# Kernel tuning notes

Hardware: AMD Instinct MI355X
Metric: run time of the kernel (lower is better)

## Reference

```python
import jax, jax.numpy as jnp
import numpy as np

N, E, E2 = 50000, 100000, 100000
NODE_IN, H, EDGE_IN, EDGE_H = 64, 32, 16, 128
STEPS = 3
ALPHA = 0.5
BETA = 1.0 / STEPS  # forward overwrites self.beta with 1/num_steps
EPS = 1e-5


def setup_inputs() -> dict:
    key = jax.random.key(0)
    ks = jax.random.split(key, 16)
    p = lambda k, shape, s=0.05: (jax.random.normal(k, shape, jnp.float32) * s)
    return {
        "n_feat": jax.random.normal(ks[0], (N, NODE_IN), jnp.float32),
        "e_feat": jax.random.normal(ks[1], (E, EDGE_IN), jnp.float32),
        "src": jax.random.randint(ks[2], (E,), 0, N, jnp.int32),
        "dst": jax.random.randint(ks[3], (E,), 0, N, jnp.int32),
        "src_list": jax.random.randint(ks[4], (E2,), 0, N, jnp.int32),
        "dst_list": jax.random.randint(ks[5], (E2,), 0, N, jnp.int32),
        "lin0_w": p(ks[6], (H, NODE_IN)), "lin0_b": jnp.zeros((H,), jnp.float32),
        "en1_w": p(ks[7], (EDGE_H, EDGE_IN)), "en1_b": jnp.zeros((EDGE_H,), jnp.float32),
        "en2_w": p(ks[8], (H * H, EDGE_H)), "en2_b": jnp.zeros((H * H,), jnp.float32),
        "conv_bias": jnp.zeros((H,), jnp.float32),
        "lin1_w": p(ks[9], (H, H)), "lin1_b": jnp.zeros((H,), jnp.float32),
        "bn_gamma": jnp.ones((H,), jnp.float32), "bn_beta": jnp.zeros((H,), jnp.float32),
        "ylin_w": p(ks[10], (3, H)), "ylin_b": jnp.zeros((3,), jnp.float32),
        "ylin2_w": p(ks[11], (1, H)), "ylin2_b": jnp.zeros((1,), jnp.float32),
    }


def reference(n_feat, e_feat, src, dst, src_list, dst_list,
              lin0_w, lin0_b, en1_w, en1_b, en2_w, en2_b, conv_bias,
              lin1_w, lin1_b, bn_gamma, bn_beta, ylin_w, ylin_b, ylin2_w, ylin2_b):
    n = n_feat.shape[0]
    out = jax.nn.relu(n_feat @ lin0_w.T + lin0_b)
    h0 = out
    # Edge-conditioned weights (eval mode: dropouts are identity, so the
    # edge MLP output is identical every step -> compute once).
    We = (jax.nn.relu(e_feat @ en1_w.T + en1_b) @ en2_w.T + en2_b).reshape(-1, H, H)  # (E,H,H)
    for _ in range(STEPS):
        msg = jnp.einsum('eh,eho->eo', out[src], We)                 # per-edge matvec
        agg = jax.ops.segment_sum(msg, dst, num_segments=n)          # sum aggregator
        conv = agg + out + conv_bias                                 # identity residual + bias
        temp = ALPHA * conv + (1.0 - ALPHA) * h0
        out = jax.nn.relu(BETA * (temp @ lin1_w.T + lin1_b) + (1.0 - BETA) * temp)
    # BatchNorm1d with batch statistics (training-mode stats, biased var)
    mu = out.mean(axis=0)
    var = ((out - mu) ** 2).mean(axis=0)
    y_bn = (out - mu) / jnp.sqrt(var + EPS) * bn_gamma + bn_beta
    y_sigmoid = jax.nn.sigmoid(y_bn @ ylin_w.T + ylin_b)                              # (N,3)
    edge_hop_out = jax.nn.sigmoid((y_bn[src_list] * y_bn[dst_list]) @ ylin2_w.T + ylin2_b)  # (E2,1)
    return (y_sigmoid, edge_hop_out)
```

## Files before the change

kernel.cpp:

```cpp
#include <hip/hip_runtime.h>
#include <hip/hip_bf16.h>
#include <math.h>

#define HH 32
#define NODE_IN 64
#define EDGE_IN 16
#define EDGE_H 128
#define M_TILE 256

typedef __attribute__((ext_vector_type(8))) short bf16x8;
typedef __attribute__((ext_vector_type(4))) float f32x4;

__device__ inline unsigned short f2bf(float f) {
    union { float f; unsigned int u; } v; v.f = f;
    unsigned int r = v.u + 0x7fff + ((v.u >> 16) & 1);
    return (unsigned short)(r >> 16);
}

__device__ inline void gload_lds16(const void* g, void* lds) {
    __builtin_amdgcn_global_load_lds(
        (const __attribute__((address_space(1))) void*)g,
        (__attribute__((address_space(3))) void*)lds, 16, 0, 0);
}

__global__ void k_prep_w2(const float* __restrict__ en2_w, unsigned short* __restrict__ W2s) {
    int i = blockIdx.x * 256 + threadIdx.x;
    int r = i >> 7, q = i & 127;
    int p = q >> 3, sub = q & 7;
    int c = p ^ (r & 15);
    W2s[i] = f2bf(en2_w[r * EDGE_H + c * 8 + sub]);
}

__global__ void __launch_bounds__(256, 4)
k_prep_r(const float* __restrict__ e_feat, const float* __restrict__ en1_w,
         const float* __restrict__ en1_b, unsigned short* __restrict__ Rb,
         int E, int E_pad) {
    int t = threadIdx.x, wave = t >> 6, l = t & 63;
    int lo = l & 15, lq = l >> 4;
    int ebase = blockIdx.x * 256 + wave * 64;

    bf16x8 bfrag[8];
    #pragma unroll
    for (int nt = 0; nt < 8; ++nt) {
        unsigned short br[8] = {0, 0, 0, 0, 0, 0, 0, 0};
        if (lq < 2) {
            const float* wr = en1_w + (nt * 16 + lo) * EDGE_IN + lq * 8;
            #pragma unroll
            for (int z = 0; z < 8; ++z) br[z] = f2bf(wr[z]);
        }
        bfrag[nt] = *(const bf16x8*)br;
    }
    float b1v[8];
    #pragma unroll
    for (int nt = 0; nt < 8; ++nt) b1v[nt] = en1_b[nt * 16 + lo];

    #pragma unroll
    for (int m = 0; m < 4; ++m) {
        int ea = ebase + m * 16 + lo;
        unsigned short ar[8] = {0, 0, 0, 0, 0, 0, 0, 0};
        if (lq < 2 && ea < E) {
            const float* er = e_feat + (size_t)ea * EDGE_IN + lq * 8;
            float4 v0 = ((const float4*)er)[0];
            float4 v1 = ((const float4*)er)[1];
            ar[0] = f2bf(v0.x); ar[1] = f2bf(v0.y); ar[2] = f2bf(v0.z); ar[3] = f2bf(v0.w);
            ar[4] = f2bf(v1.x); ar[5] = f2bf(v1.y); ar[6] = f2bf(v1.z); ar[7] = f2bf(v1.w);
        }
        bf16x8 af = *(const bf16x8*)ar;

        int erow = ebase + m * 16 + lq * 4;
        #pragma unroll
        for (int nt = 0; nt < 8; ++nt) {
            f32x4 acc = (f32x4){b1v[nt], b1v[nt], b1v[nt], b1v[nt]};
            acc = __builtin_amdgcn_mfma_f32_16x16x32_bf16(af, bfrag[nt], acc, 0, 0, 0);
            #pragma unroll
            for (int r = 0; r < 4; ++r)
                Rb[(size_t)(erow + r) * EDGE_H + nt * 16 + lo] = f2bf(fmaxf(acc[r], 0.f));
        }
    }
}

__global__ void k_lin0(const float* __restrict__ nf, const float* __restrict__ w,
                       const float* __restrict__ b, float* __restrict__ out,
                       float* __restrict__ h0, int n) {
    __shared__ float nf_s[8][NODE_IN];
    __shared__ float w_s[HH][NODE_IN + 1];
    int t = threadIdx.x;
    for (int i = t; i < HH * NODE_IN; i += 256) w_s[i / NODE_IN][i % NODE_IN] = w[i];
    int n0 = blockIdx.x * 8;
    for (int i = t; i < 8 * NODE_IN; i += 256) {
        int nl = i / NODE_IN, k = i % NODE_IN;
        int nn = n0 + nl;
        nf_s[nl][k] = (nn < n) ? nf[(size_t)nn * NODE_IN + k] : 0.f;
    }
    __syncthreads();
    int nl = t >> 5, h = t & 31;
    int nn = n0 + nl;
    if (nn < n) {
        float acc = b[h];
        #pragma unroll
        for (int k = 0; k < NODE_IN; ++k) acc += nf_s[nl][k] * w_s[h][k];
        acc = fmaxf(acc, 0.f);
        out[(size_t)nn * HH + h] = acc;
        h0[(size_t)nn * HH + h] = acc;
    }
}

__global__ void k_zero_int(int* __restrict__ p, int n) {
    int i = blockIdx.x * 256 + threadIdx.x;
    if (i < n) p[i] = 0;
}
__global__ void k_hist(const int* __restrict__ dst, int* __restrict__ deg, int E) {
    int e = blockIdx.x * 256 + threadIdx.x;
    if (e < E) atomicAdd(&deg[dst[e]], 1);
}
__global__ void k_scan1(const int* __restrict__ deg, int* __restrict__ offtmp,
                        int* __restrict__ bsum, int n) {
    __shared__ int sh[256];
    int tid = threadIdx.x;
    int i = blockIdx.x * 256 + tid;
    int v = (i < n) ? deg[i] : 0;
    sh[tid] = v;
    __syncthreads();
    for (int d = 1; d < 256; d <<= 1) {
        int add = (tid >= d) ? sh[tid - d] : 0;
        __syncthreads();
        sh[tid] += add;
        __syncthreads();
    }
    if (i < n) offtmp[i] = sh[tid] - v;
    if (tid == 255) bsum[blockIdx.x] = sh[255];
}
__global__ void k_scan2(int* __restrict__ bsum, int nb) {
    __shared__ int sh[256];
    int tid = threadIdx.x;
    int v = (tid < nb) ? bsum[tid] : 0;
    sh[tid] = v;
    __syncthreads();
    for (int d = 1; d < 256; d <<= 1) {
        int add = (tid >= d) ? sh[tid - d] : 0;
        __syncthreads();
        sh[tid] += add;
        __syncthreads();
    }
    if (tid < nb) bsum[tid] = sh[tid] - v;
}
__global__ void k_scan3(const int* __restrict__ offtmp, const int* __restrict__ bsum,
                        int* __restrict__ offsets, int* __restrict__ cursor, int n, int E) {
    int i = blockIdx.x * 256 + threadIdx.x;
    if (i < n) { offsets[i] = offtmp[i] + bsum[i >> 8]; cursor[i] = 0; }
    if (i == n) offsets[n] = E;
}
__global__ void k_scatter_pos(const int* __restrict__ dst, const int* __restrict__ offsets,
                              int* __restrict__ cursor, int* __restrict__ pos, int E) {
    int e = blockIdx.x * 256 + threadIdx.x;
    if (e < E) pos[e] = offsets[dst[e]] + atomicAdd(&cursor[dst[e]], 1);
}

__global__ void __launch_bounds__(512, 2)
k_edge_mfma4(const unsigned short* __restrict__ Rb, const unsigned short* __restrict__ W2s,
             const float* __restrict__ b2, const float* __restrict__ cur,
             const int* __restrict__ src, const int* __restrict__ pos,
             float* __restrict__ outp, int E) {
    __shared__ unsigned short w2buf[4][32 * EDGE_H];
    __shared__ float x_t[HH][M_TILE];
    __shared__ float b2_s[HH * HH];
    int t = threadIdx.x, wave = t >> 6, l = t & 63;
    int lo = l & 15, lq = l >> 4;
    int e0 = blockIdx.x * M_TILE;

    for (int i = t; i < HH * HH; i += 512) b2_s[i] = b2[i];

    for (int i = t; i < M_TILE * 8; i += 512) {
        int el = i >> 3, c = i & 7;
        int e = e0 + el;
        float4 v = make_float4(0.f, 0.f, 0.f, 0.f);
        if (e < E) v = ((const float4*)(cur + (size_t)src[e] * HH))[c];
        x_t[c * 4 + 0][el] = v.x; x_t[c * 4 + 1][el] = v.y;
        x_t[c * 4 + 2][el] = v.z; x_t[c * 4 + 3][el] = v.w;
    }

    bf16x8 afrag[2][4];
    #pragma unroll
    for (int m = 0; m < 2; ++m)
        #pragma unroll
        for (int ks = 0; ks < 4; ++ks)
            afrag[m][ks] = *(const bf16x8*)(Rb + (size_t)(e0 + wave * 32 + m * 16 + lo) * EDGE_H + ks * 32 + lq * 8);

    #pragma unroll
    for (int s = 0; s < 3; ++s)
        gload_lds16(W2s + (size_t)s * 4096 + t * 8, &w2buf[s][t * 8]);

    asm volatile("s_waitcnt lgkmcnt(0)" ::: "memory");

    float macc[2][2][4];
    #pragma unroll
    for (int m = 0; m < 2; ++m)
        #pragma unroll
        for (int nn = 0; nn < 2; ++nn)
            #pragma unroll
            for (int r = 0; r < 4; ++r) macc[m][nn][r] = 0.f;

    #pragma unroll 4
    for (int h = 0; h < HH; ++h) {
        if (h < 30)      asm volatile("s_waitcnt vmcnt(2)" ::: "memory");
        else if (h == 30) asm volatile("s_waitcnt vmcnt(1)" ::: "memory");
        else              asm volatile("s_waitcnt vmcnt(0)" ::: "memory");
        __builtin_amdgcn_s_barrier();
        if (h + 3 < HH)
            gload_lds16(W2s + (size_t)(h + 3) * 4096 + t * 8, &w2buf[(h + 3) & 3][t * 8]);

        const unsigned short* wb = w2buf[h & 3];
        bf16x8 bfrag[2][4];
        #pragma unroll
        for (int nn = 0; nn < 2; ++nn)
            #pragma unroll
            for (int ks = 0; ks < 4; ++ks)
                bfrag[nn][ks] = *(const bf16x8*)&wb[(nn * 16 + lo) * EDGE_H + (((ks * 4 + lq) ^ lo) * 8)];

        f32x4 acc[2][2];
        #pragma unroll
        for (int nn = 0; nn < 2; ++nn) {
            float bb = b2_s[h * HH + nn * 16 + lo];
            acc[0][nn] = (f32x4){bb, bb, bb, bb};
            acc[1][nn] = (f32x4){bb, bb, bb, bb};
        }
        #pragma unroll
        for (int ks = 0; ks < 4; ++ks)
            #pragma unroll
            for (int m = 0; m < 2; ++m)
                #pragma unroll
                for (int nn = 0; nn < 2; ++nn)
                    acc[m][nn] = __builtin_amdgcn_mfma_f32_16x16x32_bf16(
                        afrag[m][ks], bfrag[nn][ks], acc[m][nn], 0, 0, 0);

        #pragma unroll
        for (int m = 0; m < 2; ++m) {
            const float4 xv = *(const float4*)&x_t[h][wave * 32 + m * 16 + lq * 4];
            #pragma unroll
            for (int nn = 0; nn < 2; ++nn) {
                macc[m][nn][0] += xv.x * acc[m][nn][0];
                macc[m][nn][1] += xv.y * acc[m][nn][1];
                macc[m][nn][2] += xv.z * acc[m][nn][2];
                macc[m][nn][3] += xv.w * acc[m][nn][3];
            }
        }
    }

    #pragma unroll
    for (int m = 0; m < 2; ++m) {
        int ebase = e0 + wave * 32 + m * 16 + lq * 4;
        const int4 p4 = *(const int4*)&pos[ebase];
        int pr[4] = { p4.x, p4.y, p4.z, p4.w };
        #pragma unroll
        for (int r = 0; r < 4; ++r) {
            if (ebase + r < E) {
                outp[(size_t)pr[r] * HH + lo]      = macc[m][0][r];
                outp[(size_t)pr[r] * HH + 16 + lo] = macc[m][1][r];
            }
        }
    }
}

__global__ void k_node_update(const float* __restrict__ msg_sorted, const int* __restrict__ offsets,
                              const float* __restrict__ cur, const float* __restrict__ h0,
                              const float* __restrict__ conv_bias,
                              const float* __restrict__ lin1_w, const float* __restrict__ lin1_b,
                              float* __restrict__ nxt, int n) {
    __shared__ float t_s[8][HH + 1];
    __shared__ float w_s[HH][HH + 1];
    int t = threadIdx.x;
    for (int i = t; i < HH * HH; i += 256) w_s[i >> 5][i & 31] = lin1_w[i];
    int nl = t >> 5, h = t & 31;
    int nn = blockIdx.x * 8 + nl;
    float tv = 0.f;
    if (nn < n) {
        int s0 = offsets[nn], s1 = offsets[nn + 1];
        float s = 0.f;
        for (int i = s0; i < s1; ++i) s += msg_sorted[(size_t)i * HH + h];
        size_t idx = (size_t)nn * HH + h;
        float conv = s + cur[idx] + conv_bias[h];
        tv = 0.5f * conv + 0.5f * h0[idx];
    }
    t_s[nl][h] = tv;
    __syncthreads();
    if (nn < n) {
        const float BETA = 1.0f / 3.0f;
        float d = lin1_b[h];
        #pragma unroll
        for (int k = 0; k < HH; ++k) d += t_s[nl][k] * w_s[h][k];
        float v = BETA * d + (1.0f - BETA) * tv;
        nxt[(size_t)nn * HH + h] = fmaxf(v, 0.f);
    }
}

__global__ void k_bn_stats(const float* __restrict__ out, float* __restrict__ stats, int n) {
    int t = threadIdx.x;
    int h = t & 31, rg = t >> 5;
    float s = 0.f, s2 = 0.f;
    for (int nn = blockIdx.x * 8 + rg; nn < n; nn += gridDim.x * 8) {
        float v = out[(size_t)nn * HH + h];
        s += v; s2 += v * v;
    }
    __shared__ float sh[256], sh2[256];
    sh[t] = s; sh2[t] = s2;
    __syncthreads();
    if (rg == 0) {
        #pragma unroll
        for (int g = 1; g < 8; ++g) { s += sh[g * 32 + h]; s2 += sh2[g * 32 + h]; }
        atomicAdd(&stats[h], s);
        atomicAdd(&stats[32 + h], s2);
    }
}

__global__ void k_node_out(const float* __restrict__ out, const float* __restrict__ stats,
                           const float* __restrict__ gamma, const float* __restrict__ beta,
                           const float* __restrict__ ylin_w, const float* __restrict__ ylin_b,
                           float* __restrict__ y_bn, float* __restrict__ y_sig, int n) {
    int nn = blockIdx.x * blockDim.x + threadIdx.x;
    if (nn >= n) return;
    float inv_n = 1.f / (float)n;
    float yb[HH];
    #pragma unroll
    for (int h = 0; h < HH; ++h) {
        float mu = stats[h] * inv_n;
        float var = stats[32 + h] * inv_n - mu * mu;
        float v = out[(size_t)nn * HH + h];
        yb[h] = (v - mu) * rsqrtf(var + 1e-5f) * gamma[h] + beta[h];
    }
    #pragma unroll
    for (int h = 0; h < HH; ++h) y_bn[(size_t)nn * HH + h] = yb[h];
    #pragma unroll
    for (int c = 0; c < 3; ++c) {
        float d = ylin_b[c];
        #pragma unroll
        for (int h = 0; h < HH; ++h) d += yb[h] * ylin_w[c * HH + h];
        y_sig[(size_t)nn * 3 + c] = 1.f / (1.f + expf(-d));
    }
}

__global__ void k_edge_hop(const float* __restrict__ y_bn, const int* __restrict__ sl,
                           const int* __restrict__ dl, const float* __restrict__ w,
                           const float* __restrict__ b, float* __restrict__ outp, int e2) {
    int e = blockIdx.x * blockDim.x + threadIdx.x;
    if (e >= e2) return;
    const float4* a = (const float4*)(y_bn + (size_t)sl[e] * HH);
    const float4* c = (const float4*)(y_bn + (size_t)dl[e] * HH);
    float d = b[0];
    #pragma unroll
    for (int q = 0; q < 8; ++q) {
        float4 av = a[q], cv = c[q];
        float4 wv = ((const float4*)w)[q];
        d += av.x * cv.x * wv.x + av.y * cv.y * wv.y + av.z * cv.z * wv.z + av.w * cv.w * wv.w;
    }
    outp[e] = 1.f / (1.f + expf(-d));
}

extern "C" void kernel_launch(void* const* d_in, const int* in_sizes, int n_in,
                              void* d_out, int out_size, void* d_ws, size_t ws_size,
                              hipStream_t stream) {
    const float* n_feat   = (const float*)d_in[0];
    const float* e_feat   = (const float*)d_in[1];
    const int*   src      = (const int*)d_in[2];
    const int*   dst      = (const int*)d_in[3];
    const int*   src_list = (const int*)d_in[4];
    const int*   dst_list = (const int*)d_in[5];
    const float* lin0_w   = (const float*)d_in[6];
    const float* lin0_b   = (const float*)d_in[7];
    const float* en1_w    = (const float*)d_in[8];
    const float* en1_b    = (const float*)d_in[9];
    const float* en2_w    = (const float*)d_in[10];
    const float* en2_b    = (const float*)d_in[11];
    const float* conv_bias= (const float*)d_in[12];
    const float* lin1_w   = (const float*)d_in[13];
    const float* lin1_b   = (const float*)d_in[14];
    const float* bn_gamma = (const float*)d_in[15];
    const float* bn_beta  = (const float*)d_in[16];
    const float* ylin_w   = (const float*)d_in[17];
    const float* ylin_b   = (const float*)d_in[18];
    const float* ylin2_w  = (const float*)d_in[19];
    const float* ylin2_b  = (const float*)d_in[20];

    int n  = in_sizes[0] / NODE_IN;
    int E  = in_sizes[1] / EDGE_IN;
    int e2 = in_sizes[4];
    int E_pad = (E + M_TILE - 1) & ~(M_TILE - 1);

    float* ws    = (float*)d_ws;
    size_t nh    = (size_t)n * HH;
    float* out_a = ws;
    float* out_b = out_a + nh;
    float* h0    = out_b + nh;
    float* y_bn  = h0 + nh;
    float* stats = y_bn + nh;
    float* msg_sorted = stats + 64;
    unsigned short* W2s = (unsigned short*)(msg_sorted + (size_t)E_pad * HH);
    unsigned short* Rb  = W2s + 1024 * EDGE_H;
    int* ibase   = (int*)(Rb + (size_t)E_pad * EDGE_H);
    int* deg     = ibase;
    int* offtmp  = deg + n;
    int* bsum    = offtmp + n;
    int* offsets = bsum + 256;
    int* cursor  = offsets + n + 1;
    int* pos     = cursor + n;

    int nb = (n + 255) / 256;

    k_prep_w2<<<(1024 * EDGE_H) / 256, 256, 0, stream>>>(en2_w, W2s);
    k_prep_r<<<E_pad / 256, 256, 0, stream>>>(e_feat, en1_w, en1_b, Rb, E, E_pad);
    k_lin0<<<(n + 7) / 8, 256, 0, stream>>>(n_feat, lin0_w, lin0_b, out_a, h0, n);

    k_zero_int<<<nb, 256, 0, stream>>>(deg, n);
    k_hist<<<(E + 255) / 256, 256, 0, stream>>>(dst, deg, E);
    k_scan1<<<nb, 256, 0, stream>>>(deg, offtmp, bsum, n);
    k_scan2<<<1, 256, 0, stream>>>(bsum, nb);
    k_scan3<<<(n + 256) / 256, 256, 0, stream>>>(offtmp, bsum, offsets, cursor, n, E);
    k_scatter_pos<<<(E + 255) / 256, 256, 0, stream>>>(dst, offsets, cursor, pos, E);

    const float* cur = out_a;
    float* nxt = out_b;
    for (int s = 0; s < 3; ++s) {
        k_edge_mfma4<<<E_pad / M_TILE, 512, 0, stream>>>(
            Rb, W2s, en2_b, cur, src, pos, msg_sorted, E);
        k_node_update<<<(n + 7) / 8, 256, 0, stream>>>(
            msg_sorted, offsets, cur, h0, conv_bias, lin1_w, lin1_b, nxt, n);
        float* t = (float*)cur; cur = nxt; nxt = t;
    }

    hipMemsetAsync(stats, 0, 64 * sizeof(float), stream);
    k_bn_stats<<<256, 256, 0, stream>>>(cur, stats, n);

    float* y_sig = (float*)d_out;
    float* e_out = y_sig + (size_t)n * 3;
    k_node_out<<<(n + 255) / 256, 256, 0, stream>>>(
        cur, stats, bn_gamma, bn_beta, ylin_w, ylin_b, y_bn, y_sig, n);
    k_edge_hop<<<(e2 + 255) / 256, 256, 0, stream>>>(
        y_bn, src_list, dst_list, ylin2_w, ylin2_b, e_out, e2);
}
```

Measured before the change: 270.4 us.

## Precompute per-edge weight matrices once and aggregate with atomics

Adds a path that materializes the full per-edge HxH weight tensor in bf16 once, using a single MFMA GEMM. Each of the three steps then runs a lightweight matvec kernel that reads these matrices and scatters results with float atomics, replacing the CSR sort and histogram/scan setup. The aim is to stop recomputing the large edge GEMM every step. In exchange it writes and re-reads about 200 MB of bf16 per step, needs a much larger workspace (it falls back to the old path if the workspace is too small), and makes summation order nondeterministic.

Measured after the change: 270.6 us. Within noise of the previous version (+0.1%).

```diff
diff --git a/kernel.cpp b/kernel.cpp
--- a/kernel.cpp
+++ b/kernel.cpp
@@ -21,6 +21,15 @@
     __builtin_amdgcn_global_load_lds(
         (const __attribute__((address_space(1))) void*)g,
         (__attribute__((address_space(3))) void*)lds, 16, 0, 0);
+}
+
+__global__ void k_prep_w2p(const float* __restrict__ en2_w, unsigned short* __restrict__ W2s) {
+    int i = blockIdx.x * 256 + threadIdx.x;
+    int cp = i >> 7, q = i & 127;
+    int p = q >> 3, sub = q & 7;
+    int orow = ((cp & 31) << 5) | (cp >> 5);
+    int c = p ^ (cp & 15);
+    W2s[i] = f2bf(en2_w[orow * EDGE_H + c * 8 + sub]);
 }
 
 __global__ void k_prep_w2(const float* __restrict__ en2_w, unsigned short* __restrict__ W2s) {
@@ -102,6 +111,145 @@
         acc = fmaxf(acc, 0.f);
         out[(size_t)nn * HH + h] = acc;
         h0[(size_t)nn * HH + h] = acc;
+    }
+}
+
+__global__ void __launch_bounds__(512, 2)
+k_gemm_c(const unsigned short* __restrict__ Rb, const unsigned short* __restrict__ W2s,
+         const float* __restrict__ b2, unsigned short* __restrict__ Cb) {
+    __shared__ unsigned short w2buf[2][4 * 32 * EDGE_H];
+    __shared__ float b2p_s[1024];
+    int t = threadIdx.x, wave = t >> 6, l = t & 63;
+    int lo = l & 15, lq = l >> 4;
+    int e0 = blockIdx.x * M_TILE;
+
+    for (int i = t; i < 1024; i += 512)
+        b2p_s[i] = b2[((i & 31) << 5) | (i >> 5)];
+
+    bf16x8 afrag[2][4];
+    #pragma unroll
+    for (int m = 0; m < 2; ++m)
+        #pragma unroll
+        for (int ks = 0; ks < 4; ++ks)
+            afrag[m][ks] = *(const bf16x8*)(Rb + (size_t)(e0 + wave * 32 + m * 16 + lo) * EDGE_H + ks * 32 + lq * 8);
+
+    #pragma unroll
+    for (int k = 0; k < 4; ++k)
+        gload_lds16(W2s + k * 4096 + t * 8, &w2buf[0][k * 4096 + t * 8]);
+
+    asm volatile("s_waitcnt lgkmcnt(0)" ::: "memory");
+
+    for (int g = 0; g < 8; ++g) {
+        asm volatile("s_waitcnt vmcnt(0)" ::: "memory");
+        __builtin_amdgcn_s_barrier();
+        if (g + 1 < 8) {
+            #pragma unroll
+            for (int k = 0; k < 4; ++k)
+                gload_lds16(W2s + (size_t)(g + 1) * 16384 + k * 4096 + t * 8,
+                            &w2buf[(g + 1) & 1][k * 4096 + t * 8]);
+        }
+        const unsigned short* wb = w2buf[g & 1];
+
+        #pragma unroll
+        for (int cgl = 0; cgl < 4; ++cgl) {
+            int cg = g * 4 + cgl;
+            bf16x8 bfrag[2][4];
+            #pragma unroll
+            for (int nn = 0; nn < 2; ++nn)
+                #pragma unroll
+                for (int ks = 0; ks < 4; ++ks)
+                    bfrag[nn][ks] = *(const bf16x8*)&wb[cgl * 4096 + (nn * 16 + lo) * EDGE_H + (((ks * 4 + lq) ^ lo) * 8)];
+
+            f32x4 acc[2][2];
+            #pragma unroll
+            for (int nn = 0; nn < 2; ++nn) {
+                float bb = b2p_s[cg * 32 + nn * 16 + lo];
+                acc[0][nn] = (f32x4){bb, bb, bb, bb};
+                acc[1][nn] = (f32x4){bb, bb, bb, bb};
+            }
+            #pragma unroll
+            for (int ks = 0; ks < 4; ++ks)
+                #pragma unroll
+                for (int m = 0; m < 2; ++m)
+                    #pragma unroll
+                    for (int nn = 0; nn < 2; ++nn)
+                        acc[m][nn] = __builtin_amdgcn_mfma_f32_16x16x32_bf16(
+                            afrag[m][ks], bfrag[nn][ks], acc[m][nn], 0, 0, 0);
+
+            #pragma unroll
+            for (int m = 0; m < 2; ++m) {
+                int erow = e0 + wave * 32 + m * 16 + lq * 4;
+                #pragma unroll
+                for (int nn = 0; nn < 2; ++nn)
+                    #pragma unroll
+                    for (int r = 0; r < 4; ++r)
+                        Cb[(size_t)(erow + r) * 1024 + cg * 32 + nn * 16 + lo] = f2bf(acc[m][nn][r]);
+            }
+        }
+    }
+}
+
+__global__ void __launch_bounds__(256)
+k_step(const unsigned short* __restrict__ Cb, const float* __restrict__ cur,
+       const int* __restrict__ src, const int* __restrict__ dst,
+       float* __restrict__ agg, int E) {
+    __shared__ float x_s[8][33];
+    int t = threadIdx.x;
+    {
+        int ee = blockIdx.x * 8 + (t >> 5);
+        int h = t & 31;
+        x_s[t >> 5][h] = (ee < E) ? cur[(size_t)src[ee] * HH + h] : 0.f;
+    }
+    __syncthreads();
+    int el = t >> 5, o = t & 31;
+    int e = blockIdx.x * 8 + el;
+    if (e >= E) return;
+    const uint4* cp = (const uint4*)(Cb + (size_t)e * 1024 + o * 32);
+    const float* xr = x_s[el];
+    float s = 0.f;
+    #pragma unroll
+    for (int w4 = 0; w4 < 4; ++w4) {
+        uint4 c = cp[w4];
+        unsigned int uu[4] = {c.x, c.y, c.z, c.w};
+        #pragma unroll
+        for (int q = 0; q < 4; ++q) {
+            unsigned int u = uu[q];
+            union { unsigned int i; float f; } flo, fhi;
+            flo.i = u << 16;
+            fhi.i = u & 0xffff0000u;
+            int h = w4 * 8 + q * 2;
+            s += xr[h] * flo.f + xr[h + 1] * fhi.f;
+        }
+    }
+    atomicAdd(&agg[(size_t)dst[e] * HH + o], s);
+}
+
+__global__ void k_node_update_agg(const float* __restrict__ agg,
+                                  const float* __restrict__ cur, const float* __restrict__ h0,
+                                  const float* __restrict__ conv_bias,
+                                  const float* __restrict__ lin1_w, const float* __restrict__ lin1_b,
+                                  float* __restrict__ nxt, int n) {
+    __shared__ float t_s[8][HH + 1];
+    __shared__ float w_s[HH][HH + 1];
+    int t = threadIdx.x;
+    for (int i = t; i < HH * HH; i += 256) w_s[i >> 5][i & 31] = lin1_w[i];
+    int nl = t >> 5, h = t & 31;
+    int nn = blockIdx.x * 8 + nl;
+    float tv = 0.f;
+    if (nn < n) {
+        size_t idx = (size_t)nn * HH + h;
+        float conv = agg[idx] + cur[idx] + conv_bias[h];
+        tv = 0.5f * conv + 0.5f * h0[idx];
+    }
+    t_s[nl][h] = tv;
+    __syncthreads();
+    if (nn < n) {
+        const float BETA = 1.0f / 3.0f;
+        float d = lin1_b[h];
+        #pragma unroll
+        for (int k = 0; k < HH; ++k) d += t_s[nl][k] * w_s[h][k];
+        float v = BETA * d + (1.0f - BETA) * tv;
+        nxt[(size_t)nn * HH + h] = fmaxf(v, 0.f);
     }
 }
 
@@ -202,7 +350,7 @@
 
     #pragma unroll 4
     for (int h = 0; h < HH; ++h) {
-        if (h < 30)      asm volatile("s_waitcnt vmcnt(2)" ::: "memory");
+        if (h < 30)       asm volatile("s_waitcnt vmcnt(2)" ::: "memory");
         else if (h == 30) asm volatile("s_waitcnt vmcnt(1)" ::: "memory");
         else              asm volatile("s_waitcnt vmcnt(0)" ::: "memory");
         __builtin_amdgcn_s_barrier();
@@ -261,11 +409,11 @@
     }
 }
 
-__global__ void k_node_update(const float* __restrict__ msg_sorted, const int* __restrict__ offsets,
-                              const float* __restrict__ cur, const float* __restrict__ h0,
-                              const float* __restrict__ conv_bias,
-                              const float* __restrict__ lin1_w, const float* __restrict__ lin1_b,
-                              float* __restrict__ nxt, int n) {
+__global__ void k_node_update_csr(const float* __restrict__ msg_sorted, const int* __restrict__ offsets,
+                                  const float* __restrict__ cur, const float* __restrict__ h0,
+                                  const float* __restrict__ conv_bias,
+                                  const float* __restrict__ lin1_w, const float* __restrict__ lin1_b,
+                                  float* __restrict__ nxt, int n) {
     __shared__ float t_s[8][HH + 1];
     __shared__ float w_s[HH][HH + 1];
     int t = threadIdx.x;
@@ -385,54 +533,98 @@
     int e2 = in_sizes[4];
     int E_pad = (E + M_TILE - 1) & ~(M_TILE - 1);
 
-    float* ws    = (float*)d_ws;
-    size_t nh    = (size_t)n * HH;
-    float* out_a = ws;
-    float* out_b = out_a + nh;
-    float* h0    = out_b + nh;
-    float* y_bn  = h0 + nh;
-    float* stats = y_bn + nh;
-    float* msg_sorted = stats + 64;
-    unsigned short* W2s = (unsigned short*)(msg_sorted + (size_t)E_pad * HH);
-    unsigned short* Rb  = W2s + 1024 * EDGE_H;
-    int* ibase   = (int*)(Rb + (size_t)E_pad * EDGE_H);
-    int* deg     = ibase;
-    int* offtmp  = deg + n;
-    int* bsum    = offtmp + n;
-    int* offsets = bsum + 256;
-    int* cursor  = offsets + n + 1;
-    int* pos     = cursor + n;
-
-    int nb = (n + 255) / 256;
-
-    k_prep_w2<<<(1024 * EDGE_H) / 256, 256, 0, stream>>>(en2_w, W2s);
-    k_prep_r<<<E_pad / 256, 256, 0, stream>>>(e_feat, en1_w, en1_b, Rb, E, E_pad);
-    k_lin0<<<(n + 7) / 8, 256, 0, stream>>>(n_feat, lin0_w, lin0_b, out_a, h0, n);
-
-    k_zero_int<<<nb, 256, 0, stream>>>(deg, n);
-    k_hist<<<(E + 255) / 256, 256, 0, stream>>>(dst, deg, E);
-    k_scan1<<<nb, 256, 0, stream>>>(deg, offtmp, bsum, n);
-    k_scan2<<<1, 256, 0, stream>>>(bsum, nb);
-    k_scan3<<<(n + 256) / 256, 256, 0, stream>>>(offtmp, bsum, offsets, cursor, n, E);
-    k_scatter_pos<<<(E + 255) / 256, 256, 0, stream>>>(dst, offsets, cursor, pos, E);
-
-    const float* cur = out_a;
-    float* nxt = out_b;
-    for (int s = 0; s < 3; ++s) {
-        k_edge_mfma4<<<E_pad / M_TILE, 512, 0, stream>>>(
-            Rb, W2s, en2_b, cur, src, pos, msg_sorted, E);
-        k_node_update<<<(n + 7) / 8, 256, 0, stream>>>(
-            msg_sorted, offsets, cur, h0, conv_bias, lin1_w, lin1_b, nxt, n);
-        float* t = (float*)cur; cur = nxt; nxt = t;
-    }
-
-    hipMemsetAsync(stats, 0, 64 * sizeof(float), stream);
-    k_bn_stats<<<256, 256, 0, stream>>>(cur, stats, n);
-
-    float* y_sig = (float*)d_out;
-    float* e_out = y_sig + (size_t)n * 3;
-    k_node_out<<<(n + 255) / 256, 256, 0, stream>>>(
-        cur, stats, bn_gamma, bn_beta, ylin_w, ylin_b, y_bn, y_sig, n);
-    k_edge_hop<<<(e2 + 255) / 256, 256, 0, stream>>>(
-        y_bn, src_list, dst_list, ylin2_w, ylin2_b, e_out, e2);
-}
+    float* ws = (float*)d_ws;
+    size_t nh = (size_t)n * HH;
+
+    size_t needed = ((size_t)5 * nh + 64) * 4
+                  + (size_t)1024 * EDGE_H * 2
+                  + (size_t)E_pad * EDGE_H * 2
+                  + (size_t)E_pad * 1024 * 2;
+
+    if (ws_size >= needed) {
+        float* out_a = ws;
+        float* out_b = out_a + nh;
+        float* h0    = out_b + nh;
+        float* y_bn  = h0 + nh;
+        float* stats = y_bn + nh;
+        float* agg   = stats + 64;
+        unsigned short* W2s = (unsigned short*)(agg + nh);
+        unsigned short* Rb  = W2s + 1024 * EDGE_H;
+        unsigned short* Cb  = Rb + (size_t)E_pad * EDGE_H;
+
+        k_prep_w2p<<<(1024 * EDGE_H) / 256, 256, 0, stream>>>(en2_w, W2s);
+        k_prep_r<<<E_pad / 256, 256, 0, stream>>>(e_feat, en1_w, en1_b, Rb, E, E_pad);
+        k_lin0<<<(n + 7) / 8, 256, 0, stream>>>(n_feat, lin0_w, lin0_b, out_a, h0, n);
+
+        k_gemm_c<<<E_pad / M_TILE, 512, 0, stream>>>(Rb, W2s, en2_b, Cb);
+
+        const float* cur = out_a;
+        float* nxt = out_b;
+        for (int s = 0; s < 3; ++s) {
+            hipMemsetAsync(agg, 0, nh * sizeof(float), stream);
+            k_step<<<(E + 7) / 8, 256, 0, stream>>>(Cb, cur, src, dst, agg, E);
+            k_node_update_agg<<<(n + 7) / 8, 256, 0, stream>>>(
+                agg, cur, h0, conv_bias, lin1_w, lin1_b, nxt, n);
+            float* t = (float*)cur; cur = nxt; nxt = t;
+        }
+
+        hipMemsetAsync(stats, 0, 64 * sizeof(float), stream);
+        k_bn_stats<<<256, 256, 0, stream>>>(cur, stats, n);
+
+        float* y_sig = (float*)d_out;
+        float* e_out = y_sig + (size_t)n * 3;
+        k_node_out<<<(n + 255) / 256, 256, 0, stream>>>(
+            cur, stats, bn_gamma, bn_beta, ylin_w, ylin_b, y_bn, y_sig, n);
+        k_edge_hop<<<(e2 + 255) / 256, 256, 0, stream>>>(
+            y_bn, src_list, dst_list, ylin2_w, ylin2_b, e_out, e2);
+    } else {
+        float* out_a = ws;
+        float* out_b = out_a + nh;
+        float* h0    = out_b + nh;
+        float* y_bn  = h0 + nh;
+        float* stats = y_bn + nh;
+        float* msg_sorted = stats + 64;
+        unsigned short* W2s = (unsigned short*)(msg_sorted + (size_t)E_pad * HH);
+        unsigned short* Rb  = W2s + 1024 * EDGE_H;
+        int* ibase   = (int*)(Rb + (size_t)E_pad * EDGE_H);
+        int* deg     = ibase;
+        int* offtmp  = deg + n;
+        int* bsum    = offtmp + n;
+        int* offsets = bsum + 256;
+        int* cursor  = offsets + n + 1;
+        int* pos     = cursor + n;
+
+        int nb = (n + 255) / 256;
+
+        k_prep_w2<<<(1024 * EDGE_H) / 256, 256, 0, stream>>>(en2_w, W2s);
+        k_prep_r<<<E_pad / 256, 256, 0, stream>>>(e_feat, en1_w, en1_b, Rb, E, E_pad);
+        k_lin0<<<(n + 7) / 8, 256, 0, stream>>>(n_feat, lin0_w, lin0_b, out_a, h0, n);
+
+        k_zero_int<<<nb, 256, 0, stream>>>(deg, n);
+        k_hist<<<(E + 255) / 256, 256, 0, stream>>>(dst, deg, E);
+        k_scan1<<<nb, 256, 0, stream>>>(deg, offtmp, bsum, n);
+        k_scan2<<<1, 256, 0, stream>>>(bsum, nb);
+        k_scan3<<<(n + 256) / 256, 256, 0, stream>>>(offtmp, bsum, offsets, cursor, n, E);
+        k_scatter_pos<<<(E + 255) / 256, 256, 0, stream>>>(dst, offsets, cursor, pos, E);
+
+        const float* cur = out_a;
+        float* nxt = out_b;
+        for (int s = 0; s < 3; ++s) {
+            k_edge_mfma4<<<E_pad / M_TILE, 512, 0, stream>>>(
+                Rb, W2s, en2_b, cur, src, pos, msg_sorted, E);
+            k_node_update_csr<<<(n + 7) / 8, 256, 0, stream>>>(
+                msg_sorted, offsets, cur, h0, conv_bias, lin1_w, lin1_b, nxt, n);
+            float* t = (float*)cur; cur = nxt; nxt = t;
+        }
+
+        hipMemsetAsync(stats, 0, 64 * sizeof(float), stream);
+        k_bn_stats<<<256, 256, 0, stream>>>(cur, stats, n);
+
+        float* y_sig = (float*)d_out;
+        float* e_out = y_sig + (size_t)n * 3;
+        k_node_out<<<(n + 255) / 256, 256, 0, stream>>>(
+            cur, stats, bn_gamma, bn_beta, ylin_w, ylin_b, y_bn, y_sig, n);
+        k_edge_hop<<<(e2 + 255) / 256, 256, 0, stream>>>(
+            y_bn, src_list, dst_list, ylin2_w, ylin2_b, e_out, e2);
+    }
+}
```
